# Optimization experiments

Measured on AMD Instinct MI355X. Metric: run time of the kernel, lower is better.

## Reference

```python
import math
import jax, jax.numpy as jnp
import numpy as np

B, T, HID, H, D = 2, 2048, 1024, 16, 64
EPS = 1e-5


def score_norm(s):
    # standardize scores over the key axis (per row), as in RealFormer-style score normalization
    mu = jnp.mean(s, axis=-1, keepdims=True)
    sd = jnp.std(s, axis=-1, keepdims=True)
    return (s - mu) / (sd + EPS)


def setup_inputs() -> dict:
    key = jax.random.key(0)
    ks = jax.random.split(key, 9)
    w_scale = 1.0 / math.sqrt(HID)
    return {
        "x": jax.random.normal(ks[0], (B, T, HID), dtype=jnp.float32),
        "s_prev": jax.random.normal(ks[1], (B, H, T, T), dtype=jnp.float32),
        "Wq": jax.random.normal(ks[2], (HID, H * D), dtype=jnp.float32) * w_scale,
        "Wk": jax.random.normal(ks[3], (HID, H * D), dtype=jnp.float32) * w_scale,
        "Wv": jax.random.normal(ks[4], (HID, H * D), dtype=jnp.float32) * w_scale,
        "Wo": jax.random.normal(ks[5], (H * D, HID), dtype=jnp.float32) * w_scale,
        "alpha": jnp.zeros((H,), dtype=jnp.float32),   # alpha_init = 0.0
        "gamma": jnp.ones((H,), dtype=jnp.float32),    # gamma_init = 1.0
        "beta": jnp.zeros((H,), dtype=jnp.float32),    # beta_init = 0.0
    }


def reference(x, s_prev, Wq, Wk, Wv, Wo, alpha, gamma, beta):
    Bx, t, _ = x.shape
    # project and split heads: [B, H, t, D]
    def split(h):
        return h.reshape(Bx, t, H, D).transpose(0, 2, 1, 3)
    Q = split(x @ Wq)
    K = split(x @ Wk)
    V = split(x @ Wv)

    raw = jnp.einsum('bhtd,bhsd->bhts', Q, K) / math.sqrt(D)

    # gated residual score term (s_prev detached: residual_grad_flow=False)
    gate = jax.nn.sigmoid(alpha)[None, :, None, None]
    scale = gamma[None, :, None, None]
    shift = beta[None, :, None, None]
    r = gate * (scale * score_norm(jax.lax.stop_gradient(s_prev)) + shift)
    raw = raw + r

    # causal mask (t > 1 path)
    causal = jnp.triu(jnp.ones((t, t), dtype=bool), k=1)  # True above diagonal
    scores = jnp.where(causal[None, None], -jnp.inf, raw)

    w = jax.nn.softmax(scores, axis=-1)
    ctx = jnp.einsum('bhts,bhsd->bhtd', w, V)
    merged = ctx.transpose(0, 2, 1, 3).reshape(Bx, t, H * D)
    out = merged @ Wo
    return out, raw
```

## Files before the change

kernel.cpp:

```cpp
#include <hip/hip_runtime.h>

typedef __attribute__((ext_vector_type(4))) float f32x4;
typedef __attribute__((ext_vector_type(8))) short s16x8;
typedef __attribute__((ext_vector_type(4))) unsigned short u16x4;
typedef unsigned short ushortT;

__device__ inline ushortT f2bf(float f) {
  union { float f; unsigned u; } v; v.f = f;
  unsigned r = v.u + 0x7fffu + ((v.u >> 16) & 1u);
  return (ushortT)(r >> 16);
}
__device__ inline float bf2f(ushortT s) {
  union { unsigned u; float f; } v; v.u = ((unsigned)s) << 16;
  return v.f;
}
__device__ inline f32x4 mfma16(s16x8 a, s16x8 b, f32x4 c) {
  return __builtin_amdgcn_mfma_f32_16x16x32_bf16(a, b, c, 0, 0, 0);
}
typedef const __attribute__((address_space(1))) unsigned GU;
typedef __attribute__((address_space(3))) unsigned LU;
__device__ inline void gload_lds16(const void* g, void* l) {
  __builtin_amdgcn_global_load_lds((GU*)g, (LU*)l, 16, 0, 0);
}

__global__ void conv_bf16(const float* __restrict__ in, ushortT* __restrict__ o) {
  size_t i = ((size_t)blockIdx.x * 256 + threadIdx.x) * 4;
  f32x4 v = *(const f32x4*)(in + i);
  u16x4 u = { f2bf(v[0]), f2bf(v[1]), f2bf(v[2]), f2bf(v[3]) };
  *(u16x4*)(o + i) = u;
}

__global__ void transp_bf16(const float* __restrict__ Wm, ushortT* __restrict__ wt) {
  __shared__ float t[32][33];
  int bx = blockIdx.x, by = blockIdx.y;
  int x = threadIdx.x, y = threadIdx.y;
#pragma unroll
  for (int i = 0; i < 32; i += 8)
    t[y + i][x] = Wm[(size_t)(by * 32 + y + i) * 1024 + bx * 32 + x];
  __syncthreads();
#pragma unroll
  for (int i = 0; i < 32; i += 8)
    wt[(size_t)(bx * 32 + y + i) * 1024 + by * 32 + x] = f2bf(t[x][y + i]);
}

template <int MODE>
__global__ __launch_bounds__(256) void gemm_bt(const ushortT* __restrict__ A,
                                               const ushortT* __restrict__ Bt,
                                               ushortT* __restrict__ o0,
                                               ushortT* __restrict__ o1,
                                               ushortT* __restrict__ o2,
                                               float* __restrict__ of) {
  __shared__ ushortT lA[128 * 32];
  __shared__ ushortT lB[128 * 32];
  const int tid = threadIdx.x;
  const int w = tid >> 6, l = tid & 63;
  const int a = l & 15, hi = l >> 4;
  const int wr = w >> 1, wc = w & 1;
  const int row0 = blockIdx.y * 128, col0 = blockIdx.x * 128;
  f32x4 acc[4][4] = {};
  const int r1 = tid >> 2, c1 = tid & 3;
  const int r2 = (tid + 256) >> 2, c2 = (tid + 256) & 3;
  for (int k0 = 0; k0 < 1024; k0 += 32) {
    __syncthreads();
    gload_lds16(A + (size_t)(row0 + r1) * 1024 + k0 + c1 * 8, &lA[r1 * 32 + c1 * 8]);
    gload_lds16(A + (size_t)(row0 + r2) * 1024 + k0 + c2 * 8, &lA[r2 * 32 + c2 * 8]);
    gload_lds16(Bt + (size_t)(col0 + r1) * 1024 + k0 + c1 * 8, &lB[r1 * 32 + c1 * 8]);
    gload_lds16(Bt + (size_t)(col0 + r2) * 1024 + k0 + c2 * 8, &lB[r2 * 32 + c2 * 8]);
    __syncthreads();
    s16x8 af[4], bfr[4];
#pragma unroll
    for (int m = 0; m < 4; ++m)
      af[m] = *(const s16x8*)&lA[(wr * 64 + m * 16 + a) * 32 + hi * 8];
#pragma unroll
    for (int n = 0; n < 4; ++n)
      bfr[n] = *(const s16x8*)&lB[(wc * 64 + n * 16 + a) * 32 + hi * 8];
#pragma unroll
    for (int m = 0; m < 4; ++m)
#pragma unroll
      for (int n = 0; n < 4; ++n)
        acc[m][n] = mfma16(af[m], bfr[n], acc[m][n]);
  }
  const int proj = col0 >> 10;
#pragma unroll
  for (int m = 0; m < 4; ++m)
#pragma unroll
    for (int n = 0; n < 4; ++n) {
      const int gr0 = row0 + wr * 64 + m * 16 + hi * 4;
      const int gc = col0 + wc * 64 + n * 16 + a;
#pragma unroll
      for (int r = 0; r < 4; ++r) {
        const int gr = gr0 + r;
        float v = acc[m][n][r];
        if (MODE == 0) {
          const int bb = gr >> 11, t = gr & 2047;
          const int cc = gc & 1023;
          const int hh = cc >> 6, d = cc & 63;
          const size_t bh = (size_t)bb * 16 + hh;
          if (proj == 0)      o0[(bh * 2048 + t) * 64 + d] = f2bf(v * 0.125f);
          else if (proj == 1) o1[(bh * 2048 + t) * 64 + d] = f2bf(v);
          else                o2[(bh * 64 + d) * 2048 + t] = f2bf(v);
        } else {
          of[(size_t)gr * 1024 + gc] = v;
        }
      }
    }
}

#define SBS 2056
__global__ __launch_bounds__(512) void attn_fused(
    const ushortT* __restrict__ qw, const ushortT* __restrict__ kw,
    const ushortT* __restrict__ vtw, const float* __restrict__ sprev,
    const float* __restrict__ alpha, const float* __restrict__ gamma,
    const float* __restrict__ beta, float* __restrict__ raw,
    ushortT* __restrict__ merged) {
  __shared__ ushortT sb[16 * SBS];
  __shared__ float mu_s[16], rs_s[16], li_s[16];
  __shared__ float red[4][64][4];
  const int t0 = blockIdx.x * 16;
  const int h = blockIdx.y, b = blockIdx.z;
  const int bh = b * 16 + h;
  const int tid = threadIdx.x;
  const int w = tid >> 6, l = tid & 63;
  const int a = l & 15, hi = l >> 4;

  const ushortT* qrow = qw + ((size_t)bh * 2048 + t0 + a) * 64;
  s16x8 qf0 = *(const s16x8*)(qrow + hi * 8);
  s16x8 qf1 = *(const s16x8*)(qrow + 32 + hi * 8);

  const float* sp = sprev + ((size_t)bh * 2048 + t0) * 2048;
#pragma unroll
  for (int rr = 0; rr < 2; ++rr) {
    const int row = 2 * w + rr;
    const float* rp = sp + (size_t)row * 2048 + 4 * l;
    float sum = 0.f, sq = 0.f;
#pragma unroll
    for (int i = 0; i < 8; ++i) {
      f32x4 v = *(const f32x4*)(rp + 256 * i);
      sum += v[0] + v[1] + v[2] + v[3];
      sq += v[0] * v[0] + v[1] * v[1] + v[2] * v[2] + v[3] * v[3];
      u16x4 u = { f2bf(v[0]), f2bf(v[1]), f2bf(v[2]), f2bf(v[3]) };
      *(u16x4*)&sb[row * SBS + 4 * l + 256 * i] = u;
    }
#pragma unroll
    for (int s = 32; s >= 1; s >>= 1) {
      sum += __shfl_xor(sum, s);
      sq += __shfl_xor(sq, s);
    }
    if (l == 0) {
      float mu = sum * (1.f / 2048.f);
      float var = fmaxf(sq * (1.f / 2048.f) - mu * mu, 0.f);
      mu_s[row] = mu;
      rs_s[row] = 1.f / (sqrtf(var) + 1e-5f);
    }
  }
  const float gate = 1.f / (1.f + __expf(-alpha[h]));
  const float gm = gamma[h], bt = beta[h];
  __syncthreads();

  float mu4[4], rs4[4];
#pragma unroll
  for (int r = 0; r < 4; ++r) {
    mu4[r] = mu_s[4 * hi + r];
    rs4[r] = rs_s[4 * hi + r];
  }
  const ushortT* kb = kw + (size_t)bh * 2048 * 64;
  float* rawb = raw + ((size_t)bh * 2048 + t0) * 2048;
  for (int i = 0; i < 16; ++i) {
    const int col0 = (w + 8 * i) * 16;
    const ushortT* kr = kb + (size_t)(col0 + a) * 64 + hi * 8;
    s16x8 kf0 = *(const s16x8*)(kr);
    s16x8 kf1 = *(const s16x8*)(kr + 32);
    f32x4 s4 = {};
    s4 = mfma16(qf0, kf0, s4);
    s4 = mfma16(qf1, kf1, s4);
#pragma unroll
    for (int r = 0; r < 4; ++r) {
      const int rl = 4 * hi + r;
      const float spv = bf2f(sb[rl * SBS + col0 + a]);
      const float rv = s4[r] + gate * (gm * (spv - mu4[r]) * rs4[r] + bt);
      rawb[(size_t)rl * 2048 + col0 + a] = rv;
      sb[rl * SBS + col0 + a] = f2bf((col0 + a) <= (t0 + rl) ? rv : -1e30f);
    }
  }
  __syncthreads();

#pragma unroll
  for (int rr = 0; rr < 2; ++rr) {
    const int row = 2 * w + rr;
    float vals[32];
#pragma unroll
    for (int i = 0; i < 16; ++i) {
      unsigned u = *(const unsigned*)&sb[row * SBS + 2 * l + 128 * i];
      union { unsigned u; float f; } lo, hh;
      lo.u = u << 16; hh.u = u & 0xffff0000u;
      vals[2 * i] = lo.f; vals[2 * i + 1] = hh.f;
    }
    float m = -3e38f;
#pragma unroll
    for (int j = 0; j < 32; ++j) m = fmaxf(m, vals[j]);
#pragma unroll
    for (int s = 32; s >= 1; s >>= 1) m = fmaxf(m, __shfl_xor(m, s));
    float sum = 0.f;
#pragma unroll
    for (int j = 0; j < 32; ++j) { vals[j] = __expf(vals[j] - m); sum += vals[j]; }
#pragma unroll
    for (int s = 32; s >= 1; s >>= 1) sum += __shfl_xor(sum, s);
#pragma unroll
    for (int i = 0; i < 16; ++i) {
      unsigned u = (unsigned)f2bf(vals[2 * i]) | ((unsigned)f2bf(vals[2 * i + 1]) << 16);
      *(unsigned*)&sb[row * SBS + 2 * l + 128 * i] = u;
    }
    if (l == 0) li_s[row] = 1.f / sum;
  }
  __syncthreads();

  const int n = w & 3, half = w >> 2;
  const ushortT* vb = vtw + ((size_t)bh * 64 + 16 * n + a) * 2048;
  f32x4 acc = {};
  const int nch = (t0 + 47) >> 5;
  for (int c = half; c < nch; c += 2) {
    s16x8 pf = *(const s16x8*)&sb[a * SBS + 32 * c + 8 * hi];
    s16x8 vf = *(const s16x8*)(vb + 32 * c + 8 * hi);
    acc = mfma16(pf, vf, acc);
  }
  if (half == 1) *(f32x4*)red[n][l] = acc;
  __syncthreads();
  if (half == 0) {
    f32x4 o = *(f32x4*)red[n][l];
    acc += o;
#pragma unroll
    for (int r = 0; r < 4; ++r) {
      const int rl = 4 * hi + r;
      const float cx = acc[r] * li_s[rl];
      merged[((size_t)b * 2048 + t0 + rl) * 1024 + h * 64 + 16 * n + a] = f2bf(cx);
    }
  }
}

extern "C" void kernel_launch(void* const* d_in, const int* in_sizes, int n_in,
                              void* d_out, int out_size, void* d_ws, size_t ws_size,
                              hipStream_t stream) {
  (void)in_sizes; (void)n_in; (void)out_size; (void)ws_size;
  const float* x      = (const float*)d_in[0];
  const float* s_prev = (const float*)d_in[1];
  const float* Wq     = (const float*)d_in[2];
  const float* Wk     = (const float*)d_in[3];
  const float* Wv     = (const float*)d_in[4];
  const float* Wo     = (const float*)d_in[5];
  const float* alpha  = (const float*)d_in[6];
  const float* gamma  = (const float*)d_in[7];
  const float* beta   = (const float*)d_in[8];

  float* out = (float*)d_out;
  float* raw = out + (size_t)4194304;

  char* ws = (char*)d_ws;
  const size_t MB = 1024 * 1024;
  ushortT* xb  = (ushortT*)(ws);
  ushortT* wT  = (ushortT*)(ws + 8 * MB);
  ushortT* woT = (ushortT*)(ws + 14 * MB);
  ushortT* qw  = (ushortT*)(ws + 16 * MB);
  ushortT* kw  = (ushortT*)(ws + 24 * MB);
  ushortT* vtw = (ushortT*)(ws + 32 * MB);
  ushortT* mg  = (ushortT*)(ws + 40 * MB);

  conv_bf16<<<4096, 256, 0, stream>>>(x, xb);
  dim3 tb(32, 8);
  transp_bf16<<<dim3(32, 32), tb, 0, stream>>>(Wq, wT);
  transp_bf16<<<dim3(32, 32), tb, 0, stream>>>(Wk, wT + 1024 * 1024);
  transp_bf16<<<dim3(32, 32), tb, 0, stream>>>(Wv, wT + 2 * 1024 * 1024);
  transp_bf16<<<dim3(32, 32), tb, 0, stream>>>(Wo, woT);

  gemm_bt<0><<<dim3(24, 32), 256, 0, stream>>>(xb, wT, qw, kw, vtw, nullptr);

  attn_fused<<<dim3(128, 16, 2), 512, 0, stream>>>(qw, kw, vtw, s_prev, alpha, gamma,
                                                   beta, raw, mg);

  gemm_bt<1><<<dim3(8, 32), 256, 0, stream>>>(mg, woT, nullptr, nullptr, nullptr, out);
}
```

Measured before the change: 419.0 us.

## Shrink attention block to 8 query rows with 4 waves and packed bf16 converts

The fused attention kernel now processes 8 query rows per block with 256 threads instead of 16 rows with 512, halving LDS per block so more blocks fit per CU. The grid doubles to match. The PV stage drops its two-half split and the LDS reduction because each of the 4 waves covers one 16-column slice of D. Score normalization is folded into precomputed per-row affine coefficients, and float-to-bf16 conversion uses the hardware packed convert instruction. In exchange, half the MFMA rows are wasted because the 16-row tile holds 8 real rows, and K is reloaded by twice as many blocks.

Measured after the change: 563.5 us. 1.34x slower.

```diff
diff --git a/kernel.cpp b/kernel.cpp
--- a/kernel.cpp
+++ b/kernel.cpp
@@ -13,6 +13,11 @@
 __device__ inline float bf2f(ushortT s) {
   union { unsigned u; float f; } v; v.u = ((unsigned)s) << 16;
   return v.f;
+}
+__device__ inline unsigned pk_bf16(float lo, float hi) {
+  unsigned r;
+  asm("v_cvt_pk_bf16_f32 %0, %1, %2" : "=v"(r) : "v"(lo), "v"(hi));
+  return r;
 }
 __device__ inline f32x4 mfma16(s16x8 a, s16x8 b, f32x4 c) {
   return __builtin_amdgcn_mfma_f32_16x16x32_bf16(a, b, c, 0, 0, 0);
@@ -107,23 +112,26 @@
 }
 
 #define SBS 2056
-__global__ __launch_bounds__(512) void attn_fused(
+__global__ __launch_bounds__(256) void attn_fused(
     const ushortT* __restrict__ qw, const ushortT* __restrict__ kw,
     const ushortT* __restrict__ vtw, const float* __restrict__ sprev,
     const float* __restrict__ alpha, const float* __restrict__ gamma,
     const float* __restrict__ beta, float* __restrict__ raw,
     ushortT* __restrict__ merged) {
-  __shared__ ushortT sb[16 * SBS];
-  __shared__ float mu_s[16], rs_s[16], li_s[16];
-  __shared__ float red[4][64][4];
-  const int t0 = blockIdx.x * 16;
+  __shared__ ushortT sb[8 * SBS];
+  __shared__ float c0_s[8], c1_s[8], li_s[8];
+  const int t0 = blockIdx.x * 8;
   const int h = blockIdx.y, b = blockIdx.z;
   const int bh = b * 16 + h;
   const int tid = threadIdx.x;
   const int w = tid >> 6, l = tid & 63;
   const int a = l & 15, hi = l >> 4;
-
-  const ushortT* qrow = qw + ((size_t)bh * 2048 + t0 + a) * 64;
+  const int a8 = a & 7;
+
+  const float gate = 1.f / (1.f + __expf(-alpha[h]));
+  const float gm = gamma[h], bt = beta[h];
+
+  const ushortT* qrow = qw + ((size_t)bh * 2048 + t0 + a8) * 64;
   s16x8 qf0 = *(const s16x8*)(qrow + hi * 8);
   s16x8 qf1 = *(const s16x8*)(qrow + 32 + hi * 8);
 
@@ -138,8 +146,10 @@
       f32x4 v = *(const f32x4*)(rp + 256 * i);
       sum += v[0] + v[1] + v[2] + v[3];
       sq += v[0] * v[0] + v[1] * v[1] + v[2] * v[2] + v[3] * v[3];
-      u16x4 u = { f2bf(v[0]), f2bf(v[1]), f2bf(v[2]), f2bf(v[3]) };
-      *(u16x4*)&sb[row * SBS + 4 * l + 256 * i] = u;
+      uint2 u;
+      u.x = pk_bf16(v[0], v[1]);
+      u.y = pk_bf16(v[2], v[3]);
+      *(uint2*)&sb[row * SBS + 4 * l + 256 * i] = u;
     }
 #pragma unroll
     for (int s = 32; s >= 1; s >>= 1) {
@@ -149,37 +159,38 @@
     if (l == 0) {
       float mu = sum * (1.f / 2048.f);
       float var = fmaxf(sq * (1.f / 2048.f) - mu * mu, 0.f);
-      mu_s[row] = mu;
-      rs_s[row] = 1.f / (sqrtf(var) + 1e-5f);
-    }
-  }
-  const float gate = 1.f / (1.f + __expf(-alpha[h]));
-  const float gm = gamma[h], bt = beta[h];
-  __syncthreads();
-
-  float mu4[4], rs4[4];
+      float rs = 1.f / (sqrtf(var) + 1e-5f);
+      c1_s[row] = gate * gm * rs;
+      c0_s[row] = gate * (bt - gm * mu * rs);
+    }
+  }
+  __syncthreads();
+
+  float c04[4], c14[4];
 #pragma unroll
   for (int r = 0; r < 4; ++r) {
-    mu4[r] = mu_s[4 * hi + r];
-    rs4[r] = rs_s[4 * hi + r];
+    c04[r] = c0_s[(4 * hi + r) & 7];
+    c14[r] = c1_s[(4 * hi + r) & 7];
   }
   const ushortT* kb = kw + (size_t)bh * 2048 * 64;
   float* rawb = raw + ((size_t)bh * 2048 + t0) * 2048;
-  for (int i = 0; i < 16; ++i) {
-    const int col0 = (w + 8 * i) * 16;
+  for (int i = 0; i < 32; ++i) {
+    const int col0 = (w + 4 * i) * 16;
     const ushortT* kr = kb + (size_t)(col0 + a) * 64 + hi * 8;
     s16x8 kf0 = *(const s16x8*)(kr);
     s16x8 kf1 = *(const s16x8*)(kr + 32);
     f32x4 s4 = {};
     s4 = mfma16(qf0, kf0, s4);
     s4 = mfma16(qf1, kf1, s4);
-#pragma unroll
-    for (int r = 0; r < 4; ++r) {
-      const int rl = 4 * hi + r;
-      const float spv = bf2f(sb[rl * SBS + col0 + a]);
-      const float rv = s4[r] + gate * (gm * (spv - mu4[r]) * rs4[r] + bt);
-      rawb[(size_t)rl * 2048 + col0 + a] = rv;
-      sb[rl * SBS + col0 + a] = f2bf((col0 + a) <= (t0 + rl) ? rv : -1e30f);
+    if (hi < 2) {
+#pragma unroll
+      for (int r = 0; r < 4; ++r) {
+        const int rl = 4 * hi + r;
+        const float spv = bf2f(sb[rl * SBS + col0 + a]);
+        const float rv = fmaf(c14[r], spv, s4[r] + c04[r]);
+        rawb[(size_t)rl * 2048 + col0 + a] = rv;
+        sb[rl * SBS + col0 + a] = f2bf((col0 + a) <= (t0 + rl) ? rv : -1e30f);
+      }
     }
   }
   __syncthreads();
@@ -206,28 +217,22 @@
 #pragma unroll
     for (int s = 32; s >= 1; s >>= 1) sum += __shfl_xor(sum, s);
 #pragma unroll
-    for (int i = 0; i < 16; ++i) {
-      unsigned u = (unsigned)f2bf(vals[2 * i]) | ((unsigned)f2bf(vals[2 * i + 1]) << 16);
-      *(unsigned*)&sb[row * SBS + 2 * l + 128 * i] = u;
-    }
+    for (int i = 0; i < 16; ++i)
+      *(unsigned*)&sb[row * SBS + 2 * l + 128 * i] = pk_bf16(vals[2 * i], vals[2 * i + 1]);
     if (l == 0) li_s[row] = 1.f / sum;
   }
   __syncthreads();
 
-  const int n = w & 3, half = w >> 2;
+  const int n = w;
   const ushortT* vb = vtw + ((size_t)bh * 64 + 16 * n + a) * 2048;
   f32x4 acc = {};
-  const int nch = (t0 + 47) >> 5;
-  for (int c = half; c < nch; c += 2) {
-    s16x8 pf = *(const s16x8*)&sb[a * SBS + 32 * c + 8 * hi];
+  const int nch = (t0 + 39) >> 5;
+  for (int c = 0; c < nch; ++c) {
+    s16x8 pf = *(const s16x8*)&sb[a8 * SBS + 32 * c + 8 * hi];
     s16x8 vf = *(const s16x8*)(vb + 32 * c + 8 * hi);
     acc = mfma16(pf, vf, acc);
   }
-  if (half == 1) *(f32x4*)red[n][l] = acc;
-  __syncthreads();
-  if (half == 0) {
-    f32x4 o = *(f32x4*)red[n][l];
-    acc += o;
+  if (hi < 2) {
 #pragma unroll
     for (int r = 0; r < 4; ++r) {
       const int rl = 4 * hi + r;
@@ -273,7 +278,7 @@
 
   gemm_bt<0><<<dim3(24, 32), 256, 0, stream>>>(xb, wT, qw, kw, vtw, nullptr);
 
-  attn_fused<<<dim3(128, 16, 2), 512, 0, stream>>>(qw, kw, vtw, s_prev, alpha, gamma,
+  attn_fused<<<dim3(256, 16, 2), 256, 0, stream>>>(qw, kw, vtw, s_prev, alpha, gamma,
                                                    beta, raw, mg);
 
   gemm_bt<1><<<dim3(8, 32), 256, 0, stream>>>(mg, woT, nullptr, nullptr, nullptr, out);
```

## Make attention blocks persistent over 8 row tiles with s_prev register prefetch

Applied to the files above, without the earlier changes.

The attention kernel now launches 512 blocks, and each loops over 8 consecutive 16-row tiles of one head instead of handling a single tile. The next tile's s_prev rows are loaded into registers while the current tile does QK and raw writes, so that HBM read is overlapped. Other changes: normalization constants are folded into one FMA, conversions use packed v_cvt_pk_bf16 instructions, the softmax is done in two LDS passes instead of a 32-float register array, and syncs are lighter barriers. In exchange, register pressure rises from the 64 prefetch floats under a 4-wave occupancy hint, and the grid is smaller, so latency hiding and load balance across the causal workload may suffer.

Result: slower. 551.2 us (+31.5%).

```diff
diff --git a/kernel.cpp b/kernel.cpp
--- a/kernel.cpp
+++ b/kernel.cpp
@@ -14,6 +14,16 @@
   union { unsigned u; float f; } v; v.u = ((unsigned)s) << 16;
   return v.f;
 }
+__device__ inline unsigned pk_bf16(float lo, float hi) {
+  unsigned r;
+  asm("v_cvt_pk_bf16_f32 %0, %1, %2" : "=v"(r) : "v"(lo), "v"(hi));
+  return r;
+}
+__device__ inline ushortT cvt1_bf16(float f) {
+  unsigned r;
+  asm("v_cvt_pk_bf16_f32 %0, %1, %2" : "=v"(r) : "v"(f), "v"(f));
+  return (ushortT)r;
+}
 __device__ inline f32x4 mfma16(s16x8 a, s16x8 b, f32x4 c) {
   return __builtin_amdgcn_mfma_f32_16x16x32_bf16(a, b, c, 0, 0, 0);
 }
@@ -22,6 +32,13 @@
 __device__ inline void gload_lds16(const void* g, void* l) {
   __builtin_amdgcn_global_load_lds((GU*)g, (LU*)l, 16, 0, 0);
 }
+
+#define BARRIER_LIGHT() do {                                  \
+    __builtin_amdgcn_sched_barrier(0);                        \
+    asm volatile("s_waitcnt lgkmcnt(0)" ::: "memory");        \
+    __builtin_amdgcn_s_barrier();                             \
+    __builtin_amdgcn_sched_barrier(0);                        \
+  } while (0)
 
 __global__ void conv_bf16(const float* __restrict__ in, ushortT* __restrict__ o) {
   size_t i = ((size_t)blockIdx.x * 256 + threadIdx.x) * 4;
@@ -107,132 +124,160 @@
 }
 
 #define SBS 2056
-__global__ __launch_bounds__(512) void attn_fused(
+__global__ __launch_bounds__(512, 4) void attn_fused(
     const ushortT* __restrict__ qw, const ushortT* __restrict__ kw,
     const ushortT* __restrict__ vtw, const float* __restrict__ sprev,
     const float* __restrict__ alpha, const float* __restrict__ gamma,
     const float* __restrict__ beta, float* __restrict__ raw,
     ushortT* __restrict__ merged) {
   __shared__ ushortT sb[16 * SBS];
-  __shared__ float mu_s[16], rs_s[16], li_s[16];
+  __shared__ float c0_s[16], c1_s[16], li_s[16];
   __shared__ float red[4][64][4];
-  const int t0 = blockIdx.x * 16;
-  const int h = blockIdx.y, b = blockIdx.z;
-  const int bh = b * 16 + h;
+  const int p = blockIdx.x;
+  const int bh = p >> 4, j = p & 15;
+  const int h = bh & 15, b = bh >> 4;
   const int tid = threadIdx.x;
   const int w = tid >> 6, l = tid & 63;
   const int a = l & 15, hi = l >> 4;
 
-  const ushortT* qrow = qw + ((size_t)bh * 2048 + t0 + a) * 64;
-  s16x8 qf0 = *(const s16x8*)(qrow + hi * 8);
-  s16x8 qf1 = *(const s16x8*)(qrow + 32 + hi * 8);
-
-  const float* sp = sprev + ((size_t)bh * 2048 + t0) * 2048;
-#pragma unroll
-  for (int rr = 0; rr < 2; ++rr) {
-    const int row = 2 * w + rr;
-    const float* rp = sp + (size_t)row * 2048 + 4 * l;
-    float sum = 0.f, sq = 0.f;
-#pragma unroll
-    for (int i = 0; i < 8; ++i) {
-      f32x4 v = *(const f32x4*)(rp + 256 * i);
-      sum += v[0] + v[1] + v[2] + v[3];
-      sq += v[0] * v[0] + v[1] * v[1] + v[2] * v[2] + v[3] * v[3];
-      u16x4 u = { f2bf(v[0]), f2bf(v[1]), f2bf(v[2]), f2bf(v[3]) };
-      *(u16x4*)&sb[row * SBS + 4 * l + 256 * i] = u;
-    }
-#pragma unroll
-    for (int s = 32; s >= 1; s >>= 1) {
-      sum += __shfl_xor(sum, s);
-      sq += __shfl_xor(sq, s);
-    }
-    if (l == 0) {
-      float mu = sum * (1.f / 2048.f);
-      float var = fmaxf(sq * (1.f / 2048.f) - mu * mu, 0.f);
-      mu_s[row] = mu;
-      rs_s[row] = 1.f / (sqrtf(var) + 1e-5f);
-    }
-  }
   const float gate = 1.f / (1.f + __expf(-alpha[h]));
   const float gm = gamma[h], bt = beta[h];
-  __syncthreads();
-
-  float mu4[4], rs4[4];
-#pragma unroll
-  for (int r = 0; r < 4; ++r) {
-    mu4[r] = mu_s[4 * hi + r];
-    rs4[r] = rs_s[4 * hi + r];
+  const ushortT* kb = kw + (size_t)bh * 2048 * 64;
+  const float* spb = sprev + (size_t)bh * 2048 * 2048;
+
+  f32x4 pre[2][8];
+  {
+    const int t0 = j * 128;
+#pragma unroll
+    for (int rr = 0; rr < 2; ++rr) {
+      const float* rp = spb + (size_t)(t0 + 2 * w + rr) * 2048 + 4 * l;
+#pragma unroll
+      for (int i = 0; i < 8; ++i) pre[rr][i] = *(const f32x4*)(rp + 256 * i);
+    }
   }
-  const ushortT* kb = kw + (size_t)bh * 2048 * 64;
-  float* rawb = raw + ((size_t)bh * 2048 + t0) * 2048;
-  for (int i = 0; i < 16; ++i) {
-    const int col0 = (w + 8 * i) * 16;
-    const ushortT* kr = kb + (size_t)(col0 + a) * 64 + hi * 8;
-    s16x8 kf0 = *(const s16x8*)(kr);
-    s16x8 kf1 = *(const s16x8*)(kr + 32);
-    f32x4 s4 = {};
-    s4 = mfma16(qf0, kf0, s4);
-    s4 = mfma16(qf1, kf1, s4);
+
+  for (int it = 0; it < 8; ++it) {
+    const int t0 = j * 128 + it * 16;
+    BARRIER_LIGHT();
+
+#pragma unroll
+    for (int rr = 0; rr < 2; ++rr) {
+      const int row = 2 * w + rr;
+      float sum = 0.f, sq = 0.f;
+#pragma unroll
+      for (int i = 0; i < 8; ++i) {
+        f32x4 v = pre[rr][i];
+        sum += v[0] + v[1] + v[2] + v[3];
+        sq += v[0] * v[0] + v[1] * v[1] + v[2] * v[2] + v[3] * v[3];
+        uint2 u;
+        u.x = pk_bf16(v[0], v[1]);
+        u.y = pk_bf16(v[2], v[3]);
+        *(uint2*)&sb[row * SBS + 4 * l + 256 * i] = u;
+      }
+#pragma unroll
+      for (int s = 32; s >= 1; s >>= 1) {
+        sum += __shfl_xor(sum, s);
+        sq += __shfl_xor(sq, s);
+      }
+      if (l == 0) {
+        float mu = sum * (1.f / 2048.f);
+        float var = fmaxf(sq * (1.f / 2048.f) - mu * mu, 0.f);
+        float rs = 1.f / (sqrtf(var) + 1e-5f);
+        c1_s[row] = gate * gm * rs;
+        c0_s[row] = gate * (bt - gm * mu * rs);
+      }
+    }
+    BARRIER_LIGHT();
+
+    const ushortT* qrow = qw + ((size_t)bh * 2048 + t0 + a) * 64;
+    s16x8 qf0 = *(const s16x8*)(qrow + hi * 8);
+    s16x8 qf1 = *(const s16x8*)(qrow + 32 + hi * 8);
+    float c04[4], c14[4];
 #pragma unroll
     for (int r = 0; r < 4; ++r) {
-      const int rl = 4 * hi + r;
-      const float spv = bf2f(sb[rl * SBS + col0 + a]);
-      const float rv = s4[r] + gate * (gm * (spv - mu4[r]) * rs4[r] + bt);
-      rawb[(size_t)rl * 2048 + col0 + a] = rv;
-      sb[rl * SBS + col0 + a] = f2bf((col0 + a) <= (t0 + rl) ? rv : -1e30f);
-    }
-  }
-  __syncthreads();
-
-#pragma unroll
-  for (int rr = 0; rr < 2; ++rr) {
-    const int row = 2 * w + rr;
-    float vals[32];
-#pragma unroll
+      c04[r] = c0_s[4 * hi + r];
+      c14[r] = c1_s[4 * hi + r];
+    }
+    float* rawb = raw + ((size_t)bh * 2048 + t0) * 2048;
     for (int i = 0; i < 16; ++i) {
-      unsigned u = *(const unsigned*)&sb[row * SBS + 2 * l + 128 * i];
-      union { unsigned u; float f; } lo, hh;
-      lo.u = u << 16; hh.u = u & 0xffff0000u;
-      vals[2 * i] = lo.f; vals[2 * i + 1] = hh.f;
-    }
-    float m = -3e38f;
-#pragma unroll
-    for (int j = 0; j < 32; ++j) m = fmaxf(m, vals[j]);
-#pragma unroll
-    for (int s = 32; s >= 1; s >>= 1) m = fmaxf(m, __shfl_xor(m, s));
-    float sum = 0.f;
-#pragma unroll
-    for (int j = 0; j < 32; ++j) { vals[j] = __expf(vals[j] - m); sum += vals[j]; }
-#pragma unroll
-    for (int s = 32; s >= 1; s >>= 1) sum += __shfl_xor(sum, s);
-#pragma unroll
-    for (int i = 0; i < 16; ++i) {
-      unsigned u = (unsigned)f2bf(vals[2 * i]) | ((unsigned)f2bf(vals[2 * i + 1]) << 16);
-      *(unsigned*)&sb[row * SBS + 2 * l + 128 * i] = u;
-    }
-    if (l == 0) li_s[row] = 1.f / sum;
-  }
-  __syncthreads();
-
-  const int n = w & 3, half = w >> 2;
-  const ushortT* vb = vtw + ((size_t)bh * 64 + 16 * n + a) * 2048;
-  f32x4 acc = {};
-  const int nch = (t0 + 47) >> 5;
-  for (int c = half; c < nch; c += 2) {
-    s16x8 pf = *(const s16x8*)&sb[a * SBS + 32 * c + 8 * hi];
-    s16x8 vf = *(const s16x8*)(vb + 32 * c + 8 * hi);
-    acc = mfma16(pf, vf, acc);
-  }
-  if (half == 1) *(f32x4*)red[n][l] = acc;
-  __syncthreads();
-  if (half == 0) {
-    f32x4 o = *(f32x4*)red[n][l];
-    acc += o;
-#pragma unroll
-    for (int r = 0; r < 4; ++r) {
-      const int rl = 4 * hi + r;
-      const float cx = acc[r] * li_s[rl];
-      merged[((size_t)b * 2048 + t0 + rl) * 1024 + h * 64 + 16 * n + a] = f2bf(cx);
+      const int col0 = (w + 8 * i) * 16;
+      const ushortT* kr = kb + (size_t)(col0 + a) * 64 + hi * 8;
+      s16x8 kf0 = *(const s16x8*)(kr);
+      s16x8 kf1 = *(const s16x8*)(kr + 32);
+      f32x4 s4 = {};
+      s4 = mfma16(qf0, kf0, s4);
+      s4 = mfma16(qf1, kf1, s4);
+#pragma unroll
+      for (int r = 0; r < 4; ++r) {
+        const int rl = 4 * hi + r;
+        const float spv = bf2f(sb[rl * SBS + col0 + a]);
+        const float rv = fmaf(c14[r], spv, s4[r] + c04[r]);
+        rawb[(size_t)rl * 2048 + col0 + a] = rv;
+        sb[rl * SBS + col0 + a] = cvt1_bf16((col0 + a) <= (t0 + rl) ? rv : -1e30f);
+      }
+    }
+
+    if (it < 7) {
+      const int t0n = t0 + 16;
+#pragma unroll
+      for (int rr = 0; rr < 2; ++rr) {
+        const float* rp = spb + (size_t)(t0n + 2 * w + rr) * 2048 + 4 * l;
+#pragma unroll
+        for (int i = 0; i < 8; ++i) pre[rr][i] = *(const f32x4*)(rp + 256 * i);
+      }
+    }
+    BARRIER_LIGHT();
+
+#pragma unroll
+    for (int rr = 0; rr < 2; ++rr) {
+      const int row = 2 * w + rr;
+      float m = -3e38f;
+#pragma unroll
+      for (int i = 0; i < 16; ++i) {
+        unsigned u = *(const unsigned*)&sb[row * SBS + 2 * l + 128 * i];
+        union { unsigned u; float f; } lo, hh;
+        lo.u = u << 16; hh.u = u & 0xffff0000u;
+        m = fmaxf(m, fmaxf(lo.f, hh.f));
+      }
+#pragma unroll
+      for (int s = 32; s >= 1; s >>= 1) m = fmaxf(m, __shfl_xor(m, s));
+      float sum = 0.f;
+#pragma unroll
+      for (int i = 0; i < 16; ++i) {
+        unsigned u = *(const unsigned*)&sb[row * SBS + 2 * l + 128 * i];
+        union { unsigned u; float f; } lo, hh;
+        lo.u = u << 16; hh.u = u & 0xffff0000u;
+        float e0 = __expf(lo.f - m);
+        float e1 = __expf(hh.f - m);
+        sum += e0 + e1;
+        *(unsigned*)&sb[row * SBS + 2 * l + 128 * i] = pk_bf16(e0, e1);
+      }
+#pragma unroll
+      for (int s = 32; s >= 1; s >>= 1) sum += __shfl_xor(sum, s);
+      if (l == 0) li_s[row] = 1.f / sum;
+    }
+    BARRIER_LIGHT();
+
+    const int n = w & 3, half = w >> 2;
+    const ushortT* vb = vtw + ((size_t)bh * 64 + 16 * n + a) * 2048;
+    f32x4 acc = {};
+    const int nch = (t0 + 47) >> 5;
+    for (int c = half; c < nch; c += 2) {
+      s16x8 pf = *(const s16x8*)&sb[a * SBS + 32 * c + 8 * hi];
+      s16x8 vf = *(const s16x8*)(vb + 32 * c + 8 * hi);
+      acc = mfma16(pf, vf, acc);
+    }
+    if (half == 1) *(f32x4*)red[n][l] = acc;
+    BARRIER_LIGHT();
+    if (half == 0) {
+      f32x4 o = *(f32x4*)red[n][l];
+      acc += o;
+#pragma unroll
+      for (int r = 0; r < 4; ++r) {
+        const int rl = 4 * hi + r;
+        const float cx = acc[r] * li_s[rl];
+        merged[((size_t)b * 2048 + t0 + rl) * 1024 + h * 64 + 16 * n + a] = f2bf(cx);
+      }
     }
   }
 }
@@ -273,8 +318,8 @@
 
   gemm_bt<0><<<dim3(24, 32), 256, 0, stream>>>(xb, wT, qw, kw, vtw, nullptr);
 
-  attn_fused<<<dim3(128, 16, 2), 512, 0, stream>>>(qw, kw, vtw, s_prev, alpha, gamma,
-                                                   beta, raw, mg);
+  attn_fused<<<512, 512, 0, stream>>>(qw, kw, vtw, s_prev, alpha, gamma,
+                                      beta, raw, mg);
 
   gemm_bt<1><<<dim3(8, 32), 256, 0, stream>>>(mg, woT, nullptr, nullptr, nullptr, out);
 }
```
